# Performance work log

Hardware: AMD Instinct MI355X
Metric: run time of the kernel (lower is better)

## Reference

```python
import jax, jax.numpy as jnp
import numpy as np

DIM = 1024


def setup_inputs() -> dict:
    key = jax.random.key(0)
    ks = jax.random.split(key, 10)
    B, SQ, SKV, D = 4, 2048, 2048, DIM
    s = 1.0 / np.sqrt(D)
    return {
        "query": jax.random.normal(ks[0], (B, SQ, D), dtype=jnp.float32),
        "key_value": jax.random.normal(ks[1], (B, SKV, D), dtype=jnp.float32),
        "Wq": jax.random.normal(ks[2], (D, D), dtype=jnp.float32) * s,
        "bq": jnp.zeros((D,), dtype=jnp.float32),
        "Wk": jax.random.normal(ks[3], (D, D), dtype=jnp.float32) * s,
        "bk": jnp.zeros((D,), dtype=jnp.float32),
        "Wv": jax.random.normal(ks[4], (D, D), dtype=jnp.float32) * s,
        "bv": jnp.zeros((D,), dtype=jnp.float32),
        "Wo": jax.random.normal(ks[5], (D, D), dtype=jnp.float32) * s,
        "bo": jnp.zeros((D,), dtype=jnp.float32),
    }


def reference(query, key_value, Wq, bq, Wk, bk, Wv, bv, Wo, bo):
    # Faithful to the Keras layer: NO 1/sqrt(d) scaling, single head.
    Q = jnp.einsum("bsd,de->bse", query, Wq) + bq            # [B,Sq,D]
    K = jnp.einsum("btd,de->bte", key_value, Wk) + bk        # [B,Skv,D]
    V = jnp.einsum("btd,de->bte", key_value, Wv) + bv        # [B,Skv,D]
    scores = jnp.einsum("bse,bte->bst", Q, K)                # [B,Sq,Skv]
    attn = jax.nn.softmax(scores, axis=-1)
    ctx = jnp.einsum("bst,bte->bse", attn, V)                # [B,Sq,D]
    return jnp.einsum("bse,ef->bsf", ctx, Wo) + bo
```

## Files before the change

### kernel.cpp

```cpp
#include <hip/hip_runtime.h>
#include <cstdint>
#include <type_traits>

typedef unsigned short u16;
typedef _Float16 f16;
typedef __attribute__((ext_vector_type(8))) short    s8v;
typedef __attribute__((ext_vector_type(8))) _Float16 h8v;
typedef __attribute__((ext_vector_type(4))) float    f4v;

__device__ __forceinline__ float bf2f(u16 b) {
  unsigned int u = ((unsigned int)b) << 16;
  float f;
  __builtin_memcpy(&f, &u, 4);
  return f;
}
__device__ __forceinline__ u16 f2bf(float f) {
  unsigned int u;
  __builtin_memcpy(&u, &f, 4);
  u += 0x7fffu + ((u >> 16) & 1u);
  return (u16)(u >> 16);
}

__device__ __forceinline__ void glds16(const void* g, void* l) {
  __builtin_amdgcn_global_load_lds(
      (const __attribute__((address_space(1))) unsigned int*)g,
      (__attribute__((address_space(3))) unsigned int*)l, 16, 0, 0);
}

__device__ __forceinline__ void swz_xy(int& bx, int& by) {
  const int gx = gridDim.x;
  const int p = blockIdx.y * gx + blockIdx.x;
  bx = (p >> 3) % gx;
  by = (p & 7) + 8 * (p / (gx * 8));
}

template<bool BF, int MI, int NB, int SLOTU>
__device__ __forceinline__ void pipeK(u16* Ls,
    const u16* ga0, const u16* ga1, const u16* gb0, const u16* gb1,
    const int stA, const int stB, const int aoff, const int boff,
    const int nSub, f4v (&acc)[MI][4])
{
  using FV = typename std::conditional<BF, s8v, h8v>::type;
  auto stage = [&](int st) {
    glds16(ga0, Ls + st + stA);
    glds16(ga1, Ls + st + stA + 512);
    glds16(gb0, Ls + st + stB);
    if constexpr (NB == 2) { glds16(gb1, Ls + st + stB + 512); gb1 += 32; }
    ga0 += 32; ga1 += 32; gb0 += 32;
  };
  stage(0);
  stage(SLOTU);
  if constexpr (NB == 2) asm volatile("s_waitcnt vmcnt(4)" ::: "memory");
  else                   asm volatile("s_waitcnt vmcnt(3)" ::: "memory");
  __builtin_amdgcn_s_barrier();

  for (int s = 0; s < nSub; ++s) {
    const int sl = (s & 3) * SLOTU;
    FV af[MI], bv[4];
#pragma unroll
    for (int mi = 0; mi < MI; ++mi) af[mi] = *(const FV*)&Ls[sl + aoff + mi * 512];
#pragma unroll
    for (int ni = 0; ni < 4; ++ni)  bv[ni] = *(const FV*)&Ls[sl + boff + ni * 512];
    const bool more = (s + 2 < nSub);
    if (more) stage(((s + 2) & 3) * SLOTU);
    __builtin_amdgcn_s_setprio(1);
#pragma unroll
    for (int mi = 0; mi < MI; ++mi)
#pragma unroll
      for (int ni = 0; ni < 4; ++ni) {
        if constexpr (BF)
          acc[mi][ni] = __builtin_amdgcn_mfma_f32_16x16x32_bf16(af[mi], bv[ni], acc[mi][ni], 0, 0, 0);
        else
          acc[mi][ni] = __builtin_amdgcn_mfma_f32_16x16x32_f16(af[mi], bv[ni], acc[mi][ni], 0, 0, 0);
      }
    __builtin_amdgcn_s_setprio(0);
    if (more) {
      if constexpr (NB == 2) asm volatile("s_waitcnt vmcnt(4)" ::: "memory");
      else                   asm volatile("s_waitcnt vmcnt(3)" ::: "memory");
    } else {
      asm volatile("s_waitcnt vmcnt(0)" ::: "memory");
    }
    __builtin_amdgcn_s_barrier();
  }
}

__global__ __launch_bounds__(256)
void detect_dtype(const u16* __restrict__ q, int* __restrict__ flg)
{
  __shared__ int cbig, czero;
  if (threadIdx.x == 0) { cbig = 0; czero = 0; }
  __syncthreads();
  int b = 0, z = 0;
  for (int i = threadIdx.x; i < 4096; i += 256) {
    float v = bf2f(q[i]);
    if (!(fabsf(v) < 1e4f)) b++;
    if ((i & 1) == 0 && q[i] == 0) z++;
  }
  atomicAdd(&cbig, b);
  atomicAdd(&czero, z);
  __syncthreads();
  if (threadIdx.x == 0) flg[0] = (cbig > 64 || czero > 1600) ? 1 : 0;
}

__global__ __launch_bounds__(256)
void convert_h(const int* __restrict__ flg,
               const void* __restrict__ q, const void* __restrict__ kv,
               f16* __restrict__ qo, f16* __restrict__ kvo, long n)
{
  const void* in = blockIdx.y ? kv : q;
  f16* out = blockIdx.y ? kvo : qo;
  const long i = ((long)blockIdx.x * 256 + threadIdx.x) * 8;
  if (i >= n) return;
  h8v h;
  if (flg[0] != 0) {
    const float* p = (const float*)in + i;
    f4v f0 = *(const f4v*)p;
    f4v f1 = *(const f4v*)(p + 4);
#pragma unroll
    for (int j = 0; j < 4; ++j) {
      h[j]     = (f16)f0[j];
      h[4 + j] = (f16)f1[j];
    }
  } else {
    s8v b = *(const s8v*)((const short*)in + i);
#pragma unroll
    for (int j = 0; j < 8; ++j) h[j] = (f16)bf2f((u16)b[j]);
  }
  *(h8v*)(out + i) = h;
}

__global__ __launch_bounds__(256)
void transpose_w4(const int* __restrict__ flg,
                  const void* __restrict__ w0, const void* __restrict__ w1,
                  const void* __restrict__ w2, const void* __restrict__ w3,
                  f16* __restrict__ h0, f16* __restrict__ h1,
                  f16* __restrict__ h2, u16* __restrict__ b3, int D)
{
  __shared__ float tile[32][33];
  const int zb = blockIdx.z;
  const void* in_v = (zb == 0) ? w0 : (zb == 1) ? w1 : (zb == 2) ? w2 : w3;
  const bool i32 = (flg[0] != 0);
  const u16*   in16 = (const u16*)in_v;
  const float* in32 = (const float*)in_v;
  const int c0 = blockIdx.x * 32, r0 = blockIdx.y * 32;
  const int tx = threadIdx.x, ty = threadIdx.y;
  for (int i = ty; i < 32; i += 8) {
    const long idx = (long)(r0 + i) * D + c0 + tx;
    tile[i][tx] = i32 ? in32[idx] : bf2f(in16[idx]);
  }
  __syncthreads();
  f16* outH = (zb == 0) ? h0 : (zb == 1) ? h1 : h2;
  for (int i = ty; i < 32; i += 8) {
    const long idx = (long)(c0 + i) * D + r0 + tx;
    const float v = tile[tx][i];
    if (zb == 3) b3[idx]   = f2bf(v);
    else         outH[idx] = (f16)v;
  }
}

__global__ __launch_bounds__(512)
void gemm_proj3(const int* __restrict__ flg,
                const f16* __restrict__ Qi, const f16* __restrict__ KVi,
                const f16* __restrict__ WqT, const f16* __restrict__ WkT,
                const f16* __restrict__ WvT,
                const void* __restrict__ bq, const void* __restrict__ bk,
                const void* __restrict__ bv,
                f16* __restrict__ Qf, f16* __restrict__ Kf,
                u16* __restrict__ Vt, int M, int N, int K, int SB)
{
  __shared__ u16 Ls[65536];
  const int zb = blockIdx.z;
  const u16* A = (const u16*)((zb == 0) ? Qi : KVi);
  const u16* B = (const u16*)((zb == 0) ? WqT : (zb == 1) ? WkT : WvT);
  const void* bias = (zb == 0) ? bq : (zb == 1) ? bk : bv;
  int f_in = flg[0];
  asm volatile("" : "+v"(f_in));

  const int tid = threadIdx.x, lane = tid & 63, wave = tid >> 6;
  const int wm = wave >> 2, wn = wave & 3;
  int bx, by; swz_xy(bx, by);
  const int m0 = by * 256, n0 = bx * 256;

  const int rr  = wave * 32 + (lane >> 2);
  const int cc8 = 8 * ((lane & 3) ^ ((lane >> 3) & 3));
  const u16* ga0 = A + (long)(m0 + rr) * K + cc8;
  const u16* ga1 = ga0 + 16 * (long)K;
  const u16* gb0 = B + (long)(n0 + rr) * K + cc8;
  const u16* gb1 = gb0 + 16 * (long)K;
  const int stA = wave * 1024, stB = 8192 + wave * 1024;

  const int fr  = lane & 15;
  const int fks = 8 * (((lane >> 4) ^ (lane >> 1)) & 3);
  const int aoff = (wm * 128 + fr) * 32 + fks;
  const int boff = 8192 + (wn * 64 + fr) * 32 + fks;

  f4v acc[8][4];
#pragma unroll
  for (int i = 0; i < 8; ++i)
#pragma unroll
    for (int j = 0; j < 4; ++j) acc[i][j] = (f4v){0.f, 0.f, 0.f, 0.f};

  pipeK<false, 8, 2, 16384>(Ls, ga0, ga1, gb0, gb1, stA, stB, aoff, boff, K >> 5, acc);

  const int cr = (lane >> 4) * 4, ccl = lane & 15;
  if (zb < 2) {
    f16* out = zb ? Kf : Qf;
#pragma unroll
    for (int ni = 0; ni < 4; ++ni) {
      const int gcol = n0 + wn * 64 + ni * 16 + ccl;
      const float bvv = (f_in != 0) ? ((const float*)bias)[gcol]
                                    : bf2f(((const u16*)bias)[gcol]);
#pragma unroll
      for (int mi = 0; mi < 8; ++mi)
#pragma unroll
        for (int r = 0; r < 4; ++r) {
          const long grow = (long)(m0 + wm * 128 + mi * 16 + cr + r);
          out[grow * N + gcol] = (f16)(acc[mi][ni][r] + bvv);
        }
    }
  } else {
    u16* xw = &Ls[wave * 2176];
    const int b   = m0 / SB;
    const int s0w = (m0 % SB) + wm * 128;
    const long bbase = (long)b * (long)N * SB;
    __syncthreads();
#pragma unroll
    for (int sh = 0; sh < 2; ++sh) {
#pragma unroll
      for (int dh = 0; dh < 2; ++dh) {
#pragma unroll
        for (int nl = 0; nl < 2; ++nl) {
          const int ni = dh * 2 + nl;
          const int gcol = n0 + wn * 64 + ni * 16 + ccl;
          const float bvv = (f_in != 0) ? ((const float*)bias)[gcol]
                                        : bf2f(((const u16*)bias)[gcol]);
#pragma unroll
          for (int ml = 0; ml < 4; ++ml)
#pragma unroll
            for (int r = 0; r < 4; ++r)
              xw[(ml * 16 + cr + r) * 34 + nl * 16 + ccl] =
                  f2bf(acc[sh * 4 + ml][ni][r] + bvv);
        }
        __syncthreads();
#pragma unroll
        for (int c = 0; c < 32; ++c) {
          const int gd = n0 + wn * 64 + dh * 32 + c;
          Vt[bbase + (long)gd * SB + s0w + sh * 64 + lane] = xw[lane * 34 + c];
        }
        __syncthreads();
      }
    }
  }
}

__global__ __launch_bounds__(512)
void gemm_sc(const f16* __restrict__ A_, const f16* __restrict__ B_,
             float* __restrict__ C, int M, int N, int K,
             long sA, long sB, long sC)
{
  __shared__ u16 Ls[65536];
  const long z = blockIdx.z;
  const u16* A = (const u16*)A_ + z * sA;
  const u16* B = (const u16*)B_ + z * sB;

  const int tid = threadIdx.x, lane = tid & 63, wave = tid >> 6;
  const int wm = wave >> 2, wn = wave & 3;
  int bx, by; swz_xy(bx, by);
  const int m0 = by * 256, n0 = bx * 256;

  const int rr  = wave * 32 + (lane >> 2);
  const int cc8 = 8 * ((lane & 3) ^ ((lane >> 3) & 3));
  const u16* ga0 = A + (long)(m0 + rr) * K + cc8;
  const u16* ga1 = ga0 + 16 * (long)K;
  const u16* gb0 = B + (long)(n0 + rr) * K + cc8;
  const u16* gb1 = gb0 + 16 * (long)K;
  const int stA = wave * 1024, stB = 8192 + wave * 1024;

  const int fr  = lane & 15;
  const int fks = 8 * (((lane >> 4) ^ (lane >> 1)) & 3);
  const int aoff = (wm * 128 + fr) * 32 + fks;
  const int boff = 8192 + (wn * 64 + fr) * 32 + fks;

  f4v acc[8][4];
#pragma unroll
  for (int i = 0; i < 8; ++i)
#pragma unroll
    for (int j = 0; j < 4; ++j) acc[i][j] = (f4v){0.f, 0.f, 0.f, 0.f};

  pipeK<false, 8, 2, 16384>(Ls, ga0, ga1, gb0, gb1, stA, stB, aoff, boff, K >> 5, acc);

  const int cr = (lane >> 4) * 4, ccl = lane & 15;
  float* Cz = C + z * sC;
#pragma unroll
  for (int ni = 0; ni < 4; ++ni) {
    const int gcol = n0 + wn * 64 + ni * 16 + ccl;
#pragma unroll
    for (int mi = 0; mi < 8; ++mi)
#pragma unroll
      for (int r = 0; r < 4; ++r)
        Cz[(long)(m0 + wm * 128 + mi * 16 + cr + r) * N + gcol] = acc[mi][ni][r];
  }
}

template<bool OUT_FLAG, bool HAS_BIAS>
__global__ __launch_bounds__(512)
void gemm_bf(const int* __restrict__ flg, const u16* __restrict__ A_,
             const u16* __restrict__ Bt, const void* __restrict__ bias,
             void* __restrict__ Cv, int M, int N, int K,
             long sA, long sB, long sC)
{
  __shared__ u16 Ls[49152];
  int f_in = flg[0];
  asm volatile("" : "+v"(f_in));

  const int tid = threadIdx.x, lane = tid & 63, wave = tid >> 6;
  const int wm = wave >> 1, wn = wave & 1;
  int bx, by; swz_xy(bx, by);
  const int m0 = by * 256, n0 = bx * 128;
  const long z = blockIdx.z;
  const u16* A = A_ + z * sA;
  const u16* B = Bt + z * sB;

  const int rr  = wave * 32 + (lane >> 2);
  const int cc8 = 8 * ((lane & 3) ^ ((lane >> 3) & 3));
  const u16* ga0 = A + (long)(m0 + rr) * K + cc8;
  const u16* ga1 = ga0 + 16 * (long)K;
  const u16* gb0 = B + (long)(n0 + wave * 16 + (lane >> 2)) * K + cc8;
  const int stA = wave * 1024, stB = 8192 + wave * 512;

  const int fr  = lane & 15;
  const int fks = 8 * (((lane >> 4) ^ (lane >> 1)) & 3);
  const int aoff = (wm * 64 + fr) * 32 + fks;
  const int boff = 8192 + (wn * 64 + fr) * 32 + fks;

  f4v acc[4][4];
#pragma unroll
  for (int i = 0; i < 4; ++i)
#pragma unroll
    for (int j = 0; j < 4; ++j) acc[i][j] = (f4v){0.f, 0.f, 0.f, 0.f};

  pipeK<true, 4, 1, 12288>(Ls, ga0, ga1, gb0, gb0, stA, stB, aoff, boff, K >> 5, acc);

  const int cr = (lane >> 4) * 4, ccl = lane & 15;
  const bool o32 = OUT_FLAG && (f_in != 0);
#pragma unroll
  for (int ni = 0; ni < 4; ++ni) {
    const int gcol = n0 + wn * 64 + ni * 16 + ccl;
    float bvv = 0.f;
    if (HAS_BIAS)
      bvv = (f_in != 0) ? ((const float*)bias)[gcol] : bf2f(((const u16*)bias)[gcol]);
#pragma unroll
    for (int mi = 0; mi < 4; ++mi)
#pragma unroll
      for (int r = 0; r < 4; ++r) {
        const long grow = (long)(m0 + wm * 64 + mi * 16 + cr + r);
        const float val = acc[mi][ni][r] + bvv;
        const long idx = z * sC + grow * N + gcol;
        if (o32) ((float*)Cv)[idx] = val;
        else     ((u16*)Cv)[idx]   = f2bf(val);
      }
  }
}

__global__ __launch_bounds__(256)
void softmax_rows_bf(const float* __restrict__ S, u16* __restrict__ P, int N)
{
  const float* row = S + (long)blockIdx.x * N;
  u16* prow = P + (long)blockIdx.x * N;
  const int t = threadIdx.x;
  f4v v0 = *(const f4v*)(row + t * 8);
  f4v v1 = *(const f4v*)(row + t * 8 + 4);

  float m = v0[0];
#pragma unroll
  for (int j = 1; j < 4; ++j) m = fmaxf(m, v0[j]);
#pragma unroll
  for (int j = 0; j < 4; ++j) m = fmaxf(m, v1[j]);
  for (int off = 32; off > 0; off >>= 1) m = fmaxf(m, __shfl_down(m, off, 64));

  __shared__ float redm[4], reds[4];
  if ((t & 63) == 0) redm[t >> 6] = m;
  __syncthreads();
  m = fmaxf(fmaxf(redm[0], redm[1]), fmaxf(redm[2], redm[3]));

  float s = 0.f;
#pragma unroll
  for (int j = 0; j < 4; ++j) { v0[j] = __expf(v0[j] - m); s += v0[j]; }
#pragma unroll
  for (int j = 0; j < 4; ++j) { v1[j] = __expf(v1[j] - m); s += v1[j]; }
  for (int off = 32; off > 0; off >>= 1) s += __shfl_down(s, off, 64);
  if ((t & 63) == 0) reds[t >> 6] = s;
  __syncthreads();
  s = reds[0] + reds[1] + reds[2] + reds[3];

  const float inv = 1.f / s;
  s8v o;
#pragma unroll
  for (int j = 0; j < 4; ++j) {
    o[j]     = (short)f2bf(v0[j] * inv);
    o[4 + j] = (short)f2bf(v1[j] * inv);
  }
  *(s8v*)(prow + t * 8) = o;
}

extern "C" void kernel_launch(void* const* d_in, const int* in_sizes, int n_in,
                              void* d_out, int out_size, void* d_ws, size_t ws_size,
                              hipStream_t stream)
{
  const void* query = d_in[0];
  const void* kv    = d_in[1];
  const void* Wq    = d_in[2];
  const void* bq    = d_in[3];
  const void* Wk    = d_in[4];
  const void* bk    = d_in[5];
  const void* Wv    = d_in[6];
  const void* bv    = d_in[7];
  const void* Wo    = d_in[8];
  const void* bo    = d_in[9];

  const int Bn = 4, S = 2048, D = 1024;
  const int MS = Bn * S;
  const size_t KBu = 1024, MBu = 1024 * 1024;
  const long nTok = (long)MS * D;

  char* ws = (char*)d_ws;
  int*  flg  = (int*)(ws);
  f16*  Qi   = (f16*)(ws + 64 * KBu);
  f16*  KVi  = (f16*)(ws + 64 * KBu + 16 * MBu);
  char* rW   = ws + 64 * KBu + 32 * MBu;
  f16*  WqT  = (f16*)(rW);
  f16*  WkT  = (f16*)(rW + 2 * MBu);
  f16*  WvT  = (f16*)(rW + 4 * MBu);
  u16*  WoT  = (u16*)(rW + 6 * MBu);
  char* rQK  = rW + 8 * MBu;
  f16*  Qf   = (f16*)(rQK);
  f16*  Kf   = (f16*)(rQK + 16 * MBu);
  u16*  attn = (u16*)(rQK);
  float* Sc  = (float*)(rQK + 32 * MBu);
  char* rV   = rQK + 96 * MBu;
  u16*  Vt   = (u16*)(rV);
  u16*  Cx   = (u16*)(rV + 16 * MBu);

  detect_dtype<<<1, 256, 0, stream>>>((const u16*)query, flg);

  convert_h<<<dim3((unsigned)(nTok / 2048), 2), 256, 0, stream>>>(
      flg, query, kv, Qi, KVi, nTok);

  dim3 tb(32, 8);
  transpose_w4<<<dim3(32, 32, 4), tb, 0, stream>>>(
      flg, Wq, Wk, Wv, Wo, WqT, WkT, WvT, WoT, D);

  gemm_proj3<<<dim3(D / 256, MS / 256, 3), 512, 0, stream>>>(
      flg, Qi, KVi, WqT, WkT, WvT, bq, bk, bv, Qf, Kf, Vt, MS, D, D, S);

  gemm_sc<<<dim3(S / 256, S / 256, Bn), 512, 0, stream>>>(
      Qf, Kf, Sc, S, S, D, (long)S * D, (long)S * D, (long)S * S);
  softmax_rows_bf<<<dim3(Bn * S), 256, 0, stream>>>(Sc, attn, S);
  gemm_bf<false, false><<<dim3(D / 128, S / 256, Bn), 512, 0, stream>>>(
      flg, attn, Vt, nullptr, Cx, S, D, S, (long)S * S, (long)D * S, (long)S * D);

  gemm_bf<true, true><<<dim3(D / 128, MS / 256, 1), 512, 0, stream>>>(
      flg, Cx, WoT, bo, d_out, MS, D, D, 0L, 0L, 0L);
}
```

Before: 354.1 us.

## Replace GEMM K-pipeline with 8-phase double-buffered 64-wide K tiles

Replaces the shared pipeK main loop with pipe8, which loads 64-wide K tiles into two LDS buffers with an XOR swizzle. Each tile is split into four phases that interleave half-tile global-to-LDS loads with fragment reads and MFMA blocks, separated by barriers. The bf16 GEMMs (attn·V and the output projection) move from 256x128 to 256x256 tiles, and launch bounds request 2 blocks per CU. The aim is to hide global load latency more finely and cut LDS and global traffic per FLOP. In exchange there are more barriers per tile, higher register pressure, and fewer blocks for the smaller GEMMs.

```diff
diff --git a/kernel.cpp b/kernel.cpp
--- a/kernel.cpp
+++ b/kernel.cpp
@@ -1,6 +1,5 @@
 #include <hip/hip_runtime.h>
 #include <cstdint>
-#include <type_traits>
 
 typedef unsigned short u16;
 typedef _Float16 f16;
@@ -34,55 +33,123 @@
   by = (p & 7) + 8 * (p / (gx * 8));
 }
 
-template<bool BF, int MI, int NB, int SLOTU>
-__device__ __forceinline__ void pipeK(u16* Ls,
-    const u16* ga0, const u16* ga1, const u16* gb0, const u16* gb1,
-    const int stA, const int stB, const int aoff, const int boff,
-    const int nSub, f4v (&acc)[MI][4])
-{
-  using FV = typename std::conditional<BF, s8v, h8v>::type;
-  auto stage = [&](int st) {
-    glds16(ga0, Ls + st + stA);
-    glds16(ga1, Ls + st + stA + 512);
-    glds16(gb0, Ls + st + stB);
-    if constexpr (NB == 2) { glds16(gb1, Ls + st + stB + 512); gb1 += 32; }
-    ga0 += 32; ga1 += 32; gb0 += 32;
+template<bool BF> struct FVsel;
+template<> struct FVsel<false> {
+  using T = h8v;
+  static __device__ __forceinline__ f4v mf(T a, T b, f4v c) {
+    return __builtin_amdgcn_mfma_f32_16x16x32_f16(a, b, c, 0, 0, 0);
+  }
+};
+template<> struct FVsel<true> {
+  using T = s8v;
+  static __device__ __forceinline__ f4v mf(T a, T b, f4v c) {
+    return __builtin_amdgcn_mfma_f32_16x16x32_bf16(a, b, c, 0, 0, 0);
+  }
+};
+
+#define NOCHK ((void)0)
+#define CHK4 do { if (lastIt) asm volatile("s_waitcnt vmcnt(0)" ::: "memory"); \
+                  else        asm volatile("s_waitcnt vmcnt(4)" ::: "memory"); } while (0)
+
+#define PHASE(MH, LOADA, NH, LOADB, SLOT, CHKV)                               \
+  {                                                                           \
+    if (LOADA) {                                                              \
+      _Pragma("unroll")                                                       \
+      for (int i_ = 0; i_ < 4; ++i_) {                                        \
+        const int ro_ = bc + aFr + ((MH) * 4 + i_) * 1024;                    \
+        af0[i_] = *(const FV*)&Ls[ro_ + k0];                                  \
+        af1[i_] = *(const FV*)&Ls[ro_ + k1];                                  \
+      }                                                                       \
+    }                                                                         \
+    if (LOADB) {                                                              \
+      _Pragma("unroll")                                                       \
+      for (int i_ = 0; i_ < 2; ++i_) {                                        \
+        const int ro_ = bc + bFr + ((NH) * 2 + i_) * 1024;                    \
+        bq0[NH][i_] = *(const FV*)&Ls[ro_ + k0];                              \
+        bq1[NH][i_] = *(const FV*)&Ls[ro_ + k1];                              \
+      }                                                                       \
+    }                                                                         \
+    SLOT;                                                                     \
+    asm volatile("s_waitcnt lgkmcnt(8)" ::: "memory");                        \
+    asm volatile("s_barrier" ::: "memory");                                   \
+    asm volatile("s_waitcnt lgkmcnt(0)" ::: "memory");                        \
+    __builtin_amdgcn_s_setprio(1);                                            \
+    _Pragma("unroll")                                                         \
+    for (int i_ = 0; i_ < 4; ++i_) {                                          \
+      acc[(MH)*4+i_][(NH)*2+0] = FVsel<BF>::mf(af0[i_], bq0[NH][0], acc[(MH)*4+i_][(NH)*2+0]); \
+      acc[(MH)*4+i_][(NH)*2+1] = FVsel<BF>::mf(af0[i_], bq0[NH][1], acc[(MH)*4+i_][(NH)*2+1]); \
+      acc[(MH)*4+i_][(NH)*2+0] = FVsel<BF>::mf(af1[i_], bq1[NH][0], acc[(MH)*4+i_][(NH)*2+0]); \
+      acc[(MH)*4+i_][(NH)*2+1] = FVsel<BF>::mf(af1[i_], bq1[NH][1], acc[(MH)*4+i_][(NH)*2+1]); \
+    }                                                                         \
+    __builtin_amdgcn_s_setprio(0);                                            \
+    CHKV;                                                                     \
+    asm volatile("s_barrier" ::: "memory");                                   \
+  }
+
+template<bool BF>
+__device__ __forceinline__ void pipe8(u16* __restrict__ Ls,
+    const u16* __restrict__ A, const u16* __restrict__ B,
+    int m0, int n0, const long K, const int nT, f4v (&acc)[8][4])
+{
+  using FV = typename FVsel<BF>::T;
+  const int tid = threadIdx.x, lane = tid & 63, wave = tid >> 6;
+  const int wm = wave >> 2, wn = wave & 3;
+
+  const int jrow = tid >> 3;
+  const int cswz = ((tid & 7) ^ (jrow & 7)) << 3;
+  const u16* gA = A + (long)(m0 + jrow) * K + cswz;
+  const u16* gB = B + (long)(n0 + jrow) * K + cswz;
+  const int ldw = wave * 512;
+
+  const int fr = lane & 15, q = lane >> 4, s7 = fr & 7;
+  const int k0 = ((q ^ s7) << 3), k1 = (((q ^ 4) ^ s7) << 3);
+  const int aFr = (wm * 128 + fr) << 6;
+  const int bFr = 16384 + ((wn * 64 + fr) << 6);
+
+  auto slotA = [&](int h, int tile) {
+    if (tile < nT) {
+      u16* l = Ls + ((tile & 1) << 15) + (h << 12) + ldw;
+      const u16* g = gA + (long)(h * 64) * K + (long)tile * 64;
+      glds16(g, l);
+      glds16(g + 128 * K, l + 8192);
+    }
   };
-  stage(0);
-  stage(SLOTU);
-  if constexpr (NB == 2) asm volatile("s_waitcnt vmcnt(4)" ::: "memory");
-  else                   asm volatile("s_waitcnt vmcnt(3)" ::: "memory");
-  __builtin_amdgcn_s_barrier();
-
-  for (int s = 0; s < nSub; ++s) {
-    const int sl = (s & 3) * SLOTU;
-    FV af[MI], bv[4];
-#pragma unroll
-    for (int mi = 0; mi < MI; ++mi) af[mi] = *(const FV*)&Ls[sl + aoff + mi * 512];
-#pragma unroll
-    for (int ni = 0; ni < 4; ++ni)  bv[ni] = *(const FV*)&Ls[sl + boff + ni * 512];
-    const bool more = (s + 2 < nSub);
-    if (more) stage(((s + 2) & 3) * SLOTU);
-    __builtin_amdgcn_s_setprio(1);
-#pragma unroll
-    for (int mi = 0; mi < MI; ++mi)
-#pragma unroll
-      for (int ni = 0; ni < 4; ++ni) {
-        if constexpr (BF)
-          acc[mi][ni] = __builtin_amdgcn_mfma_f32_16x16x32_bf16(af[mi], bv[ni], acc[mi][ni], 0, 0, 0);
-        else
-          acc[mi][ni] = __builtin_amdgcn_mfma_f32_16x16x32_f16(af[mi], bv[ni], acc[mi][ni], 0, 0, 0);
-      }
-    __builtin_amdgcn_s_setprio(0);
-    if (more) {
-      if constexpr (NB == 2) asm volatile("s_waitcnt vmcnt(4)" ::: "memory");
-      else                   asm volatile("s_waitcnt vmcnt(3)" ::: "memory");
-    } else {
-      asm volatile("s_waitcnt vmcnt(0)" ::: "memory");
+  auto slotB = [&](int h, int tile) {
+    if (tile < nT) {
+      u16* l = Ls + ((tile & 1) << 15) + 16384 + (h << 12) + ldw;
+      const u16* g = gB + (long)(h * 64) * K + (long)tile * 64;
+      glds16(g, l);
+      glds16(g + 128 * K, l + 8192);
     }
-    __builtin_amdgcn_s_barrier();
-  }
-}
+  };
+
+  slotA(0, 0); slotB(0, 0); slotA(1, 0); slotB(1, 0);
+  slotA(0, 1); slotB(0, 1);
+  asm volatile("s_waitcnt vmcnt(4)" ::: "memory");
+  asm volatile("s_barrier" ::: "memory");
+
+  FV af0[4], af1[4];
+  FV bq0[2][2], bq1[2][2];
+
+  const int nIt = nT >> 1;
+  for (int t = 0; t < nIt; ++t) {
+    const int T = 2 * t;
+    const bool lastIt = (t == nIt - 1);
+    int bc = 0;
+    PHASE(0, true,  0, true,  slotA(1, T + 1), NOCHK)
+    PHASE(0, false, 1, true,  slotB(1, T + 1), NOCHK)
+    PHASE(1, true,  0, false, slotA(0, T + 2), NOCHK)
+    PHASE(1, false, 1, false, slotB(0, T + 2), CHK4)
+    bc = 32768;
+    PHASE(0, true,  0, true,  slotA(1, T + 2), NOCHK)
+    PHASE(0, false, 1, true,  slotB(1, T + 2), NOCHK)
+    PHASE(1, true,  0, false, slotA(0, T + 3), NOCHK)
+    PHASE(1, false, 1, false, slotB(0, T + 3), CHK4)
+  }
+}
+#undef PHASE
+#undef CHK4
+#undef NOCHK
 
 __global__ __launch_bounds__(256)
 void detect_dtype(const u16* __restrict__ q, int* __restrict__ flg)
@@ -158,7 +225,7 @@
   }
 }
 
-__global__ __launch_bounds__(512)
+__global__ __launch_bounds__(512, 2)
 void gemm_proj3(const int* __restrict__ flg,
                 const f16* __restrict__ Qi, const f16* __restrict__ KVi,
                 const f16* __restrict__ WqT, const f16* __restrict__ WkT,
@@ -166,7 +233,7 @@
                 const void* __restrict__ bq, const void* __restrict__ bk,
                 const void* __restrict__ bv,
                 f16* __restrict__ Qf, f16* __restrict__ Kf,
-                u16* __restrict__ Vt, int M, int N, int K, int SB)
+                u16* __restrict__ Vt, int N, int K, int SB)
 {
   __shared__ u16 Ls[65536];
   const int zb = blockIdx.z;
@@ -176,33 +243,21 @@
   int f_in = flg[0];
   asm volatile("" : "+v"(f_in));
 
-  const int tid = threadIdx.x, lane = tid & 63, wave = tid >> 6;
-  const int wm = wave >> 2, wn = wave & 3;
   int bx, by; swz_xy(bx, by);
   const int m0 = by * 256, n0 = bx * 256;
 
-  const int rr  = wave * 32 + (lane >> 2);
-  const int cc8 = 8 * ((lane & 3) ^ ((lane >> 3) & 3));
-  const u16* ga0 = A + (long)(m0 + rr) * K + cc8;
-  const u16* ga1 = ga0 + 16 * (long)K;
-  const u16* gb0 = B + (long)(n0 + rr) * K + cc8;
-  const u16* gb1 = gb0 + 16 * (long)K;
-  const int stA = wave * 1024, stB = 8192 + wave * 1024;
-
-  const int fr  = lane & 15;
-  const int fks = 8 * (((lane >> 4) ^ (lane >> 1)) & 3);
-  const int aoff = (wm * 128 + fr) * 32 + fks;
-  const int boff = 8192 + (wn * 64 + fr) * 32 + fks;
-
   f4v acc[8][4];
 #pragma unroll
   for (int i = 0; i < 8; ++i)
 #pragma unroll
     for (int j = 0; j < 4; ++j) acc[i][j] = (f4v){0.f, 0.f, 0.f, 0.f};
 
-  pipeK<false, 8, 2, 16384>(Ls, ga0, ga1, gb0, gb1, stA, stB, aoff, boff, K >> 5, acc);
-
+  pipe8<false>(Ls, A, B, m0, n0, K, K >> 6, acc);
+
+  const int lane = threadIdx.x & 63, wave = threadIdx.x >> 6;
+  const int wm = wave >> 2, wn = wave & 3;
   const int cr = (lane >> 4) * 4, ccl = lane & 15;
+
   if (zb < 2) {
     f16* out = zb ? Kf : Qf;
 #pragma unroll
@@ -223,7 +278,6 @@
     const int b   = m0 / SB;
     const int s0w = (m0 % SB) + wm * 128;
     const long bbase = (long)b * (long)N * SB;
-    __syncthreads();
 #pragma unroll
     for (int sh = 0; sh < 2; ++sh) {
 #pragma unroll
@@ -253,9 +307,9 @@
   }
 }
 
-__global__ __launch_bounds__(512)
+__global__ __launch_bounds__(512, 2)
 void gemm_sc(const f16* __restrict__ A_, const f16* __restrict__ B_,
-             float* __restrict__ C, int M, int N, int K,
+             float* __restrict__ C, int N, int K,
              long sA, long sB, long sC)
 {
   __shared__ u16 Ls[65536];
@@ -263,32 +317,19 @@
   const u16* A = (const u16*)A_ + z * sA;
   const u16* B = (const u16*)B_ + z * sB;
 
-  const int tid = threadIdx.x, lane = tid & 63, wave = tid >> 6;
-  const int wm = wave >> 2, wn = wave & 3;
   int bx, by; swz_xy(bx, by);
   const int m0 = by * 256, n0 = bx * 256;
 
-  const int rr  = wave * 32 + (lane >> 2);
-  const int cc8 = 8 * ((lane & 3) ^ ((lane >> 3) & 3));
-  const u16* ga0 = A + (long)(m0 + rr) * K + cc8;
-  const u16* ga1 = ga0 + 16 * (long)K;
-  const u16* gb0 = B + (long)(n0 + rr) * K + cc8;
-  const u16* gb1 = gb0 + 16 * (long)K;
-  const int stA = wave * 1024, stB = 8192 + wave * 1024;
-
-  const int fr  = lane & 15;
-  const int fks = 8 * (((lane >> 4) ^ (lane >> 1)) & 3);
-  const int aoff = (wm * 128 + fr) * 32 + fks;
-  const int boff = 8192 + (wn * 64 + fr) * 32 + fks;
-
   f4v acc[8][4];
 #pragma unroll
   for (int i = 0; i < 8; ++i)
 #pragma unroll
     for (int j = 0; j < 4; ++j) acc[i][j] = (f4v){0.f, 0.f, 0.f, 0.f};
 
-  pipeK<false, 8, 2, 16384>(Ls, ga0, ga1, gb0, gb1, stA, stB, aoff, boff, K >> 5, acc);
-
+  pipe8<false>(Ls, A, B, m0, n0, K, K >> 6, acc);
+
+  const int lane = threadIdx.x & 63, wave = threadIdx.x >> 6;
+  const int wm = wave >> 2, wn = wave & 3;
   const int cr = (lane >> 4) * 4, ccl = lane & 15;
   float* Cz = C + z * sC;
 #pragma unroll
@@ -303,44 +344,33 @@
 }
 
 template<bool OUT_FLAG, bool HAS_BIAS>
-__global__ __launch_bounds__(512)
+__global__ __launch_bounds__(512, 2)
 void gemm_bf(const int* __restrict__ flg, const u16* __restrict__ A_,
              const u16* __restrict__ Bt, const void* __restrict__ bias,
-             void* __restrict__ Cv, int M, int N, int K,
+             void* __restrict__ Cv, int N, int K,
              long sA, long sB, long sC)
 {
-  __shared__ u16 Ls[49152];
+  __shared__ u16 Ls[65536];
   int f_in = flg[0];
   asm volatile("" : "+v"(f_in));
 
-  const int tid = threadIdx.x, lane = tid & 63, wave = tid >> 6;
-  const int wm = wave >> 1, wn = wave & 1;
-  int bx, by; swz_xy(bx, by);
-  const int m0 = by * 256, n0 = bx * 128;
   const long z = blockIdx.z;
   const u16* A = A_ + z * sA;
   const u16* B = Bt + z * sB;
 
-  const int rr  = wave * 32 + (lane >> 2);
-  const int cc8 = 8 * ((lane & 3) ^ ((lane >> 3) & 3));
-  const u16* ga0 = A + (long)(m0 + rr) * K + cc8;
-  const u16* ga1 = ga0 + 16 * (long)K;
-  const u16* gb0 = B + (long)(n0 + wave * 16 + (lane >> 2)) * K + cc8;
-  const int stA = wave * 1024, stB = 8192 + wave * 512;
-
-  const int fr  = lane & 15;
-  const int fks = 8 * (((lane >> 4) ^ (lane >> 1)) & 3);
-  const int aoff = (wm * 64 + fr) * 32 + fks;
-  const int boff = 8192 + (wn * 64 + fr) * 32 + fks;
-
-  f4v acc[4][4];
-#pragma unroll
-  for (int i = 0; i < 4; ++i)
+  int bx, by; swz_xy(bx, by);
+  const int m0 = by * 256, n0 = bx * 256;
+
+  f4v acc[8][4];
+#pragma unroll
+  for (int i = 0; i < 8; ++i)
 #pragma unroll
     for (int j = 0; j < 4; ++j) acc[i][j] = (f4v){0.f, 0.f, 0.f, 0.f};
 
-  pipeK<true, 4, 1, 12288>(Ls, ga0, ga1, gb0, gb0, stA, stB, aoff, boff, K >> 5, acc);
-
+  pipe8<true>(Ls, A, B, m0, n0, K, K >> 6, acc);
+
+  const int lane = threadIdx.x & 63, wave = threadIdx.x >> 6;
+  const int wm = wave >> 2, wn = wave & 3;
   const int cr = (lane >> 4) * 4, ccl = lane & 15;
   const bool o32 = OUT_FLAG && (f_in != 0);
 #pragma unroll
@@ -350,10 +380,10 @@
     if (HAS_BIAS)
       bvv = (f_in != 0) ? ((const float*)bias)[gcol] : bf2f(((const u16*)bias)[gcol]);
 #pragma unroll
-    for (int mi = 0; mi < 4; ++mi)
+    for (int mi = 0; mi < 8; ++mi)
 #pragma unroll
       for (int r = 0; r < 4; ++r) {
-        const long grow = (long)(m0 + wm * 64 + mi * 16 + cr + r);
+        const long grow = (long)(m0 + wm * 128 + mi * 16 + cr + r);
         const float val = acc[mi][ni][r] + bvv;
         const long idx = z * sC + grow * N + gcol;
         if (o32) ((float*)Cv)[idx] = val;
@@ -451,14 +481,14 @@
       flg, Wq, Wk, Wv, Wo, WqT, WkT, WvT, WoT, D);
 
   gemm_proj3<<<dim3(D / 256, MS / 256, 3), 512, 0, stream>>>(
-      flg, Qi, KVi, WqT, WkT, WvT, bq, bk, bv, Qf, Kf, Vt, MS, D, D, S);
+      flg, Qi, KVi, WqT, WkT, WvT, bq, bk, bv, Qf, Kf, Vt, D, D, S);
 
   gemm_sc<<<dim3(S / 256, S / 256, Bn), 512, 0, stream>>>(
-      Qf, Kf, Sc, S, S, D, (long)S * D, (long)S * D, (long)S * S);
+      Qf, Kf, Sc, S, D, (long)S * D, (long)S * D, (long)S * S);
   softmax_rows_bf<<<dim3(Bn * S), 256, 0, stream>>>(Sc, attn, S);
-  gemm_bf<false, false><<<dim3(D / 128, S / 256, Bn), 512, 0, stream>>>(
-      flg, attn, Vt, nullptr, Cx, S, D, S, (long)S * S, (long)D * S, (long)S * D);
-
-  gemm_bf<true, true><<<dim3(D / 128, MS / 256, 1), 512, 0, stream>>>(
-      flg, Cx, WoT, bo, d_out, MS, D, D, 0L, 0L, 0L);
-}
+  gemm_bf<false, false><<<dim3(D / 256, S / 256, Bn), 512, 0, stream>>>(
+      flg, attn, Vt, nullptr, Cx, D, S, (long)S * S, (long)D * S, (long)S * D);
+
+  gemm_bf<true, true><<<dim3(D / 256, MS / 256, 1), 512, 0, stream>>>(
+      flg, Cx, WoT, bo, d_out, D, D, 0L, 0L, 0L);
+}
```

New measurement: 397.1 us. +12.1%, slower.
